# Kernel optimization log

Hardware: AMD Instinct MI355X
Metric: run time of the kernel (lower is better)

The kernel has to match this reference:

```python
import jax, jax.numpy as jnp
import numpy as np

N = 50000        # nodes
E = 250000       # edges (avg degree 5)
D = 32           # embed_dim
N_LAYERS = 3


def _uniform(key, shape, fan_in):
    s = 1.0 / np.sqrt(fan_in)
    return jax.random.uniform(key, shape, jnp.float32, -s, s)


def setup_inputs() -> dict:
    key = jax.random.key(0)
    ks = jax.random.split(key, 10)
    x = jax.random.normal(ks[0], (N, 1), jnp.float32)
    edge_index = jax.random.randint(ks[1], (2, E), 0, N, dtype=jnp.int64)
    edge_attribute = jax.random.normal(ks[2], (E, 1), jnp.float32)
    # Linear weights stored as [in, out] (i.e. torch weight transposed)
    node_W = _uniform(ks[3], (1, D), 1)
    node_b = _uniform(ks[4], (D,), 1)
    l1_W = _uniform(ks[5], (1, D * D), 1)
    l1_b = _uniform(ks[6], (D * D,), 1)
    root = _uniform(ks[7], (D, D), D)      # NNConv root weight
    conv_b = _uniform(ks[8], (D,), D)      # NNConv bias
    return {
        "x": x, "edge_index": edge_index, "edge_attribute": edge_attribute,
        "i": 2, "dummy": 0,
        "node_W": node_W, "node_b": node_b,
        "l1_W": l1_W, "l1_b": l1_b,
        "root": root, "conv_b": conv_b,
    }


def reference(x, edge_index, edge_attribute, i, dummy, node_W, node_b,
              l1_W, l1_b, root, conv_b):
    n_encode_layers = min(i + 1, N_LAYERS)
    src, dst = edge_index[0], edge_index[1]

    # node embedding: [N,1] -> [N,D]
    h = x @ node_W + node_b

    # edge-conditioned weight matrices, shared by every layer: [E, D, D]
    We = (edge_attribute @ l1_W + l1_b).reshape(E, D, D)

    # mean-aggregation denominator (in-degree, clamped; isolated nodes -> 0 msg)
    cnt = jax.ops.segment_sum(jnp.ones((E,), h.dtype), dst, num_segments=N)
    cnt = jnp.maximum(cnt, 1.0)[:, None]

    for _ in range(n_encode_layers):
        h = jax.nn.relu(h)
        # gather source features, per-edge matmul: msg_e = x_src[e] @ We[e]
        msg = jnp.einsum('ei,eio->eo', h[src], We)
        aggr = jax.ops.segment_sum(msg, dst, num_segments=N) / cnt
        h = aggr + h @ root + conv_b
    return h
```

## Files before the change

### kernel.cpp

```cpp
#include <hip/hip_runtime.h>
#include <hip/hip_bf16.h>

#define N_NODES 50000
#define N_EDGES 250000
#define DIM 32
#define BLK 256
#define CAP 64
#define SPILL_MAX 4096
#define EDGE_NB 977
#define HR_NB 6250
#define WCONV_NB 13
#define LAYER_NB 1563
#define POISON 0xAAAAAAAAu

typedef __attribute__((ext_vector_type(8))) short short8;
typedef __attribute__((ext_vector_type(4))) float f32x4;

__device__ __forceinline__ float ldf(const void* p, int i, int isf32) {
    return isf32 ? ((const float*)p)[i]
                 : __bfloat162float(((const __hip_bfloat16*)p)[i]);
}
__device__ __forceinline__ int ldi(const int* ei, int i, int i64) {
    return i64 ? ei[2 * i] : ei[i];
}
__device__ __forceinline__ int clamp_idx(int v) {
    v = v < 0 ? 0 : v;
    return v >= N_NODES ? N_NODES - 1 : v;
}
__device__ __forceinline__ bool half_is_big(const void* p, int k) {
    unsigned short h = ((const unsigned short*)p)[k];
    float v = __uint_as_float(((unsigned int)h) << 16);
    return !(fabsf(v) <= 50.0f);
}
__device__ __forceinline__ unsigned short bf16bits(float v) {
    __hip_bfloat16 b = __float2bfloat16(v);
    return __builtin_bit_cast(unsigned short, b);
}

__global__ __launch_bounds__(BLK) void prep_kernel(
    const int* __restrict__ ei, const void* __restrict__ ea,
    const void* __restrict__ x, const void* __restrict__ nW,
    const void* __restrict__ nb,
    const void* __restrict__ lW, const void* __restrict__ lb,
    const void* __restrict__ rt, const void* __restrict__ cb,
    int* __restrict__ cntI, int2* __restrict__ packed,
    int* __restrict__ spill_cnt, int4* __restrict__ spill,
    float* __restrict__ hrA, float* __restrict__ wCB,
    unsigned short* __restrict__ wfrag)
{
    __shared__ int sdet;
    int tid = threadIdx.x;
    int b = blockIdx.x;
    if (tid == 0) sdet = 0;
    __syncthreads();

    if (b < EDGE_NB) {
        if (tid < 64) {
            if (ei[2 * tid + 1] != 0) atomicOr(&sdet, 2);
        } else if (tid < 192) {
            if (half_is_big(ea, tid - 64)) atomicOr(&sdet, 1);
        }
        __syncthreads();
        int f_ea = sdet & 1, i64 = ((sdet & 2) == 0);
        int e = b * BLK + tid;
        if (e < N_EDGES) {
            int s = clamp_idx(ldi(ei, e, i64));
            int d = clamp_idx(ldi(ei, N_EDGES + e, i64));
            float a = ldf(ea, e, f_ea);
            unsigned k = (unsigned)atomicAdd(&cntI[d], 1) - POISON;
            if (k < CAP) {
                packed[d * CAP + (int)k] = make_int2(s, __float_as_int(a));
            } else {
                unsigned sp = (unsigned)atomicAdd(spill_cnt, 1) - POISON;
                if (sp < SPILL_MAX)
                    spill[sp] = make_int4(d, s, __float_as_int(a), 0);
            }
        }
        return;
    }

    if (b < EDGE_NB + HR_NB) {
        if (tid < 128) {
            if (half_is_big(x, tid)) atomicOr(&sdet, 4);
        } else if (tid < 160) {
            if (half_is_big(nW, tid - 128)) atomicOr(&sdet, 8);
        } else if (tid < 192) {
            if (half_is_big(nb, tid - 160)) atomicOr(&sdet, 16);
        }
        __syncthreads();
        int f_x = sdet & 4, f_nW = sdet & 8, f_nb = sdet & 16;
        int g = (b - EDGE_NB) * BLK + tid;
        if (g < N_NODES * DIM) {
            int n = g >> 5, dd = g & 31;
            float hv = fmaf(ldf(x, n, f_x), ldf(nW, dd, f_nW), ldf(nb, dd, f_nb));
            hrA[g] = hv > 0.0f ? hv : 0.0f;
        }
        return;
    }

    if (tid < 64)       { if (half_is_big(lW, tid) || half_is_big(lW, tid + 64)) atomicOr(&sdet, 1); }
    else if (tid < 128) { int k = tid - 64;  if (half_is_big(lb, k) || half_is_big(lb, k + 64)) atomicOr(&sdet, 2); }
    else if (tid < 192) { int k = tid - 128; if (half_is_big(rt, k) || half_is_big(rt, k + 64)) atomicOr(&sdet, 4); }
    else if (tid < 224) { if (half_is_big(cb, tid - 192)) atomicOr(&sdet, 8); }
    __syncthreads();
    int fW = sdet & 1, fB = sdet & 2, fR = sdet & 4, fC = sdet & 8;
    int g = (int)(b - EDGE_NB - HR_NB) * BLK + tid;
    if (g < 3072) {
        int f = g >> 9, rem = g & 511;
        int ln = rem >> 3, j = rem & 7;
        int t = f >> 1, nh = f & 1;
        int k = t * 32 + (ln >> 4) * 8 + j;
        int n = nh * 16 + (ln & 15);
        float v;
        if (k < 32)      v = ldf(lW, k * 32 + n, fW);
        else if (k < 64) v = ldf(lb, (k - 32) * 32 + n, fB);
        else             v = ldf(rt, (k - 64) * 32 + n, fR);
        wfrag[g] = bf16bits(v);
    } else if (g < 3104) {
        wCB[g - 3072] = ldf(cb, g - 3072, fC);
    }
}

__global__ __launch_bounds__(512) void layer_kernel(
    const int2* __restrict__ packed, const int* __restrict__ cntI,
    const int* __restrict__ spill_cnt, const int4* __restrict__ spill,
    const float* __restrict__ hin, const float* __restrict__ wCB,
    const unsigned short* __restrict__ wfrag,
    float* __restrict__ outb, int last)
{
    __shared__ __align__(16) unsigned short sAu[32 * 96];
    int tid = threadIdx.x;
    int wv = tid >> 6;
    int lane = tid & 63;
    int half = lane >> 5;
    int l32 = lane & 31;
    int nbase = blockIdx.x * 32;
    int n0 = nbase + wv * 4;

    int deg[4];
    #pragma unroll
    for (int j = 0; j < 4; ++j) {
        int n = n0 + j;
        deg[j] = (n < N_NODES) ? (int)((unsigned)cntI[n] - POISON) : 0;
    }

    float hl01 = hin[n0 * DIM + lane];
    float hl23 = hin[(n0 + 2) * DIM + lane];

    int2 c[4][4];
    #pragma unroll
    for (int j = 0; j < 4; ++j) {
        int base = (n0 + j) * CAP;
        #pragma unroll
        for (int i = 0; i < 4; ++i)
            c[j][i] = packed[base + 2 * i + half];
    }
    float h[4][4];
    #pragma unroll
    for (int j = 0; j < 4; ++j) {
        #pragma unroll
        for (int i = 0; i < 4; ++i) {
            int src = ((2 * i + half) < deg[j]) ? c[j][i].x : 0;
            h[j][i] = hin[src * DIM + l32];
        }
    }
    float p[4] = {0, 0, 0, 0}, q[4] = {0, 0, 0, 0};
    #pragma unroll
    for (int j = 0; j < 4; ++j) {
        #pragma unroll
        for (int i = 0; i < 4; ++i) {
            bool valid = (2 * i + half) < deg[j];
            float hv = valid ? h[j][i] : 0.0f;
            float a  = valid ? __int_as_float(c[j][i].y) : 0.0f;
            p[j] = fmaf(a, hv, p[j]);
            q[j] += hv;
        }
    }
    #pragma unroll
    for (int j = 0; j < 4; ++j) {
        int dgc = deg[j] < CAP ? deg[j] : CAP;
        for (int k = 8 + half; k < dgc; k += 2) {
            int2 cc = packed[(n0 + j) * CAP + k];
            float hv = hin[cc.x * DIM + l32];
            p[j] = fmaf(__int_as_float(cc.y), hv, p[j]);
            q[j] += hv;
        }
    }
    unsigned spt = (unsigned)(*spill_cnt) - POISON;
    if (spt != 0) {
        if (spt > SPILL_MAX) spt = SPILL_MAX;
        #pragma unroll
        for (int j = 0; j < 4; ++j) {
            if (deg[j] > CAP) {
                for (unsigned t = (unsigned)half; t < spt; t += 2) {
                    int4 sp = spill[t];
                    if (sp.x == n0 + j) {
                        float hv = hin[sp.y * DIM + l32];
                        p[j] = fmaf(__int_as_float(sp.z), hv, p[j]);
                        q[j] += hv;
                    }
                }
            }
        }
    }
    #pragma unroll
    for (int j = 0; j < 4; ++j) {
        p[j] += __shfl_xor(p[j], 32);
        q[j] += __shfl_xor(q[j], 32);
        float ic = 1.0f / (deg[j] < 1 ? 1.0f : (float)deg[j]);
        p[j] *= ic;
        q[j] *= ic;
    }
    #pragma unroll
    for (int j = 0; j < 4; ++j)
        sAu[(wv * 4 + j) * 96 + half * 32 + l32] = bf16bits(half ? q[j] : p[j]);
    sAu[(wv * 4 + half) * 96 + 64 + l32] = bf16bits(hl01);
    sAu[(wv * 4 + 2 + half) * 96 + 64 + l32] = bf16bits(hl23);
    __syncthreads();

    if (wv < 4) {
        int rg = wv & 1, nh = wv >> 1;
        short8 bfr[3];
        #pragma unroll
        for (int t = 0; t < 3; ++t)
            bfr[t] = *(const short8*)(wfrag + ((t * 2 + nh) * 64 + lane) * 8);
        f32x4 acc = {0.0f, 0.0f, 0.0f, 0.0f};
        #pragma unroll
        for (int t = 0; t < 3; ++t) {
            short8 afr = *(const short8*)(sAu + (rg * 16 + (lane & 15)) * 96
                                          + t * 32 + (lane >> 4) * 8);
            acc = __builtin_amdgcn_mfma_f32_16x16x32_bf16(afr, bfr[t], acc, 0, 0, 0);
        }
        float cbl = wCB[nh * 16 + (lane & 15)];
        #pragma unroll
        for (int r = 0; r < 4; ++r) {
            int row = rg * 16 + (lane >> 4) * 4 + r;
            int n = nbase + row;
            if (n < N_NODES) {
                float v = acc[r] + cbl;
                if (!last) v = v > 0.0f ? v : 0.0f;
                outb[n * DIM + nh * 16 + (lane & 15)] = v;
            }
        }
    }
}

extern "C" void kernel_launch(void* const* d_in, const int* in_sizes, int n_in,
                              void* d_out, int out_size, void* d_ws, size_t ws_size,
                              hipStream_t stream) {
    const void* p[16];
    int np_ = 0;
    for (int i = 0; i < n_in && np_ < 16; ++i)
        if (in_sizes[i] != 1) p[np_++] = d_in[i];

    const void* x      = p[0];
    const int*  ei     = (const int*)p[1];
    const void* ea     = p[2];
    const void* node_W = p[3];
    const void* node_b = p[4];
    const void* l1_W   = p[5];
    const void* l1_b   = p[6];
    const void* root   = p[7];
    const void* conv_b = p[8];
    float* out = (float*)d_out;

    const int ND = N_NODES * DIM;
    float* ws = (float*)d_ws;
    int2*  packed    = (int2*)ws;
    float* hrA       = (float*)(packed + N_NODES * CAP);
    float* hrB       = hrA + ND;
    float* wCB       = hrB + ND;
    unsigned short* wfrag = (unsigned short*)(wCB + 32);
    int*   cntI      = (int*)(wfrag + 3072);
    int*   spill_cnt = cntI + N_NODES;
    int4*  spill     = (int4*)(spill_cnt + 3);

    prep_kernel<<<EDGE_NB + HR_NB + WCONV_NB, BLK, 0, stream>>>(
        ei, ea, x, node_W, node_b, l1_W, l1_b, root, conv_b,
        cntI, packed, spill_cnt, spill, hrA, wCB, wfrag);

    layer_kernel<<<LAYER_NB, 512, 0, stream>>>(packed, cntI, spill_cnt, spill,
                                               hrA, wCB, wfrag, hrB, 0);
    layer_kernel<<<LAYER_NB, 512, 0, stream>>>(packed, cntI, spill_cnt, spill,
                                               hrB, wCB, wfrag, hrA, 0);
    layer_kernel<<<LAYER_NB, 512, 0, stream>>>(packed, cntI, spill_cnt, spill,
                                               hrA, wCB, wfrag, out, 1);
}
```

Before: 149.2 us.

## Fuse node embedding into first layer kernel and halve adjacency bucket capacity

Drops the prep stage that wrote the ReLU'd node embedding for all nodes. The first layer instead recomputes x*node_W+node_b with ReLU on the fly for each gathered source and for its own nodes, which removes a full N×D write and read. The per-node adjacency bucket capacity also shrinks from 64 to 32, cutting the packed buffer footprint. In exchange, the first layer does extra scalar loads of x plus format detection per block, and high-degree nodes fall into the spill path sooner.

```diff
diff --git a/kernel.cpp b/kernel.cpp
--- a/kernel.cpp
+++ b/kernel.cpp
@@ -5,10 +5,9 @@
 #define N_EDGES 250000
 #define DIM 32
 #define BLK 256
-#define CAP 64
+#define CAP 32
 #define SPILL_MAX 4096
 #define EDGE_NB 977
-#define HR_NB 6250
 #define WCONV_NB 13
 #define LAYER_NB 1563
 #define POISON 0xAAAAAAAAu
@@ -39,14 +38,11 @@
 
 __global__ __launch_bounds__(BLK) void prep_kernel(
     const int* __restrict__ ei, const void* __restrict__ ea,
-    const void* __restrict__ x, const void* __restrict__ nW,
-    const void* __restrict__ nb,
     const void* __restrict__ lW, const void* __restrict__ lb,
     const void* __restrict__ rt, const void* __restrict__ cb,
     int* __restrict__ cntI, int2* __restrict__ packed,
     int* __restrict__ spill_cnt, int4* __restrict__ spill,
-    float* __restrict__ hrA, float* __restrict__ wCB,
-    unsigned short* __restrict__ wfrag)
+    float* __restrict__ wCB, unsigned short* __restrict__ wfrag)
 {
     __shared__ int sdet;
     int tid = threadIdx.x;
@@ -79,32 +75,13 @@
         return;
     }
 
-    if (b < EDGE_NB + HR_NB) {
-        if (tid < 128) {
-            if (half_is_big(x, tid)) atomicOr(&sdet, 4);
-        } else if (tid < 160) {
-            if (half_is_big(nW, tid - 128)) atomicOr(&sdet, 8);
-        } else if (tid < 192) {
-            if (half_is_big(nb, tid - 160)) atomicOr(&sdet, 16);
-        }
-        __syncthreads();
-        int f_x = sdet & 4, f_nW = sdet & 8, f_nb = sdet & 16;
-        int g = (b - EDGE_NB) * BLK + tid;
-        if (g < N_NODES * DIM) {
-            int n = g >> 5, dd = g & 31;
-            float hv = fmaf(ldf(x, n, f_x), ldf(nW, dd, f_nW), ldf(nb, dd, f_nb));
-            hrA[g] = hv > 0.0f ? hv : 0.0f;
-        }
-        return;
-    }
-
     if (tid < 64)       { if (half_is_big(lW, tid) || half_is_big(lW, tid + 64)) atomicOr(&sdet, 1); }
     else if (tid < 128) { int k = tid - 64;  if (half_is_big(lb, k) || half_is_big(lb, k + 64)) atomicOr(&sdet, 2); }
     else if (tid < 192) { int k = tid - 128; if (half_is_big(rt, k) || half_is_big(rt, k + 64)) atomicOr(&sdet, 4); }
     else if (tid < 224) { if (half_is_big(cb, tid - 192)) atomicOr(&sdet, 8); }
     __syncthreads();
     int fW = sdet & 1, fB = sdet & 2, fR = sdet & 4, fC = sdet & 8;
-    int g = (int)(b - EDGE_NB - HR_NB) * BLK + tid;
+    int g = (int)(b - EDGE_NB) * BLK + tid;
     if (g < 3072) {
         int f = g >> 9, rem = g & 511;
         int ln = rem >> 3, j = rem & 7;
@@ -124,11 +101,14 @@
 __global__ __launch_bounds__(512) void layer_kernel(
     const int2* __restrict__ packed, const int* __restrict__ cntI,
     const int* __restrict__ spill_cnt, const int4* __restrict__ spill,
+    const void* __restrict__ x, const void* __restrict__ nW,
+    const void* __restrict__ nb,
     const float* __restrict__ hin, const float* __restrict__ wCB,
     const unsigned short* __restrict__ wfrag,
-    float* __restrict__ outb, int last)
+    float* __restrict__ outb, int mode0, int last)
 {
     __shared__ __align__(16) unsigned short sAu[32 * 96];
+    __shared__ int sdet;
     int tid = threadIdx.x;
     int wv = tid >> 6;
     int lane = tid & 63;
@@ -137,6 +117,24 @@
     int nbase = blockIdx.x * 32;
     int n0 = nbase + wv * 4;
 
+    float nWl = 0.0f, nbl = 0.0f;
+    int f_x = 0;
+    if (mode0) {
+        if (tid == 0) sdet = 0;
+        __syncthreads();
+        if (tid < 128) {
+            if (half_is_big(x, tid)) atomicOr(&sdet, 4);
+        } else if (tid < 160) {
+            if (half_is_big(nW, tid - 128)) atomicOr(&sdet, 8);
+        } else if (tid < 192) {
+            if (half_is_big(nb, tid - 160)) atomicOr(&sdet, 16);
+        }
+        __syncthreads();
+        f_x = sdet & 4;
+        nWl = ldf(nW, l32, sdet & 8);
+        nbl = ldf(nb, l32, sdet & 16);
+    }
+
     int deg[4];
     #pragma unroll
     for (int j = 0; j < 4; ++j) {
@@ -144,8 +142,16 @@
         deg[j] = (n < N_NODES) ? (int)((unsigned)cntI[n] - POISON) : 0;
     }
 
-    float hl01 = hin[n0 * DIM + lane];
-    float hl23 = hin[(n0 + 2) * DIM + lane];
+    float hl01, hl23;
+    if (mode0) {
+        int na = clamp_idx(n0 + half), nc = clamp_idx(n0 + 2 + half);
+        float xa = ldf(x, na, f_x), xc = ldf(x, nc, f_x);
+        hl01 = fmaf(xa, nWl, nbl); hl01 = hl01 > 0.0f ? hl01 : 0.0f;
+        hl23 = fmaf(xc, nWl, nbl); hl23 = hl23 > 0.0f ? hl23 : 0.0f;
+    } else {
+        hl01 = hin[n0 * DIM + lane];
+        hl23 = hin[(n0 + 2) * DIM + lane];
+    }
 
     int2 c[4][4];
     #pragma unroll
@@ -161,7 +167,13 @@
         #pragma unroll
         for (int i = 0; i < 4; ++i) {
             int src = ((2 * i + half) < deg[j]) ? c[j][i].x : 0;
-            h[j][i] = hin[src * DIM + l32];
+            if (mode0) {
+                float xs = ldf(x, src, f_x);
+                float hv = fmaf(xs, nWl, nbl);
+                h[j][i] = hv > 0.0f ? hv : 0.0f;
+            } else {
+                h[j][i] = hin[src * DIM + l32];
+            }
         }
     }
     float p[4] = {0, 0, 0, 0}, q[4] = {0, 0, 0, 0};
@@ -181,7 +193,14 @@
         int dgc = deg[j] < CAP ? deg[j] : CAP;
         for (int k = 8 + half; k < dgc; k += 2) {
             int2 cc = packed[(n0 + j) * CAP + k];
-            float hv = hin[cc.x * DIM + l32];
+            float hv;
+            if (mode0) {
+                float xs = ldf(x, cc.x, f_x);
+                hv = fmaf(xs, nWl, nbl);
+                hv = hv > 0.0f ? hv : 0.0f;
+            } else {
+                hv = hin[cc.x * DIM + l32];
+            }
             p[j] = fmaf(__int_as_float(cc.y), hv, p[j]);
             q[j] += hv;
         }
@@ -195,7 +214,14 @@
                 for (unsigned t = (unsigned)half; t < spt; t += 2) {
                     int4 sp = spill[t];
                     if (sp.x == n0 + j) {
-                        float hv = hin[sp.y * DIM + l32];
+                        float hv;
+                        if (mode0) {
+                            float xs = ldf(x, sp.y, f_x);
+                            hv = fmaf(xs, nWl, nbl);
+                            hv = hv > 0.0f ? hv : 0.0f;
+                        } else {
+                            hv = hin[sp.y * DIM + l32];
+                        }
                         p[j] = fmaf(__int_as_float(sp.z), hv, p[j]);
                         q[j] += hv;
                     }
@@ -267,22 +293,22 @@
     const int ND = N_NODES * DIM;
     float* ws = (float*)d_ws;
     int2*  packed    = (int2*)ws;
-    float* hrA       = (float*)(packed + N_NODES * CAP);
-    float* hrB       = hrA + ND;
-    float* wCB       = hrB + ND;
+    float* hr1       = (float*)(packed + N_NODES * CAP);
+    float* hr2       = hr1 + ND;
+    float* wCB       = hr2 + ND;
     unsigned short* wfrag = (unsigned short*)(wCB + 32);
     int*   cntI      = (int*)(wfrag + 3072);
     int*   spill_cnt = cntI + N_NODES;
     int4*  spill     = (int4*)(spill_cnt + 3);
 
-    prep_kernel<<<EDGE_NB + HR_NB + WCONV_NB, BLK, 0, stream>>>(
-        ei, ea, x, node_W, node_b, l1_W, l1_b, root, conv_b,
-        cntI, packed, spill_cnt, spill, hrA, wCB, wfrag);
+    prep_kernel<<<EDGE_NB + WCONV_NB, BLK, 0, stream>>>(
+        ei, ea, l1_W, l1_b, root, conv_b,
+        cntI, packed, spill_cnt, spill, wCB, wfrag);
 
     layer_kernel<<<LAYER_NB, 512, 0, stream>>>(packed, cntI, spill_cnt, spill,
-                                               hrA, wCB, wfrag, hrB, 0);
+        x, node_W, node_b, hr2 , wCB, wfrag, hr1, 1, 0);
     layer_kernel<<<LAYER_NB, 512, 0, stream>>>(packed, cntI, spill_cnt, spill,
-                                               hrB, wCB, wfrag, hrA, 0);
+        x, node_W, node_b, hr1, wCB, wfrag, hr2, 0, 0);
     layer_kernel<<<LAYER_NB, 512, 0, stream>>>(packed, cntI, spill_cnt, spill,
-                                               hrA, wCB, wfrag, out, 1);
-}
+        x, node_W, node_b, hr2, wCB, wfrag, out, 0, 1);
+}
```

Measured after the change: 149.1 us, median of 2. Within noise of the previous version (-0.1%).
